# Performance work log

Measured on AMD Instinct MI355X. Metric: run time of the kernel, lower is better.

## Reference

```python
import jax, jax.numpy as jnp
import numpy as np

ANCHORS = np.array([[10,13],[16,30],[33,23],[30,61],[62,45],[59,119],[116,90],[156,198],[373,326]], dtype=np.float32)
STRIDES = [32, 16, 8]
GROUPS = [2, 1, 0]  # anchor_masks [[6,7,8],[3,4,5],[0,1,2]] -> group index = mask[0]//3
N_CLASSES = 80
IGNORE_THRESH = 0.7


def _safe_log(x):
    # replicates torch BCELoss log clamp at -100, NaN-safe under grad
    ok = x > 0
    return jnp.where(ok, jnp.log(jnp.where(ok, x, 1.0)), -100.0)


def _bce_sum(o, t, w=None):
    l = -(t * _safe_log(o) + (1.0 - t) * _safe_log(1.0 - o))
    if w is not None:
        l = l * w
    return jnp.sum(l)


def _layer_loss(raw, labels, stride, group):
    dtype = raw.dtype
    B, C, H, W = raw.shape
    nch = 5 + N_CLASSES
    A = 3
    fsize = H
    T = labels.shape[1]
    all_grid = jnp.asarray(ANCHORS).astype(dtype) / stride          # [9,2] anchors in grid units
    manch = all_grid[3 * group:3 * group + 3]                        # [3,2]

    # ---- make_pred ----
    o = raw.reshape(B, A, nch, H, W).transpose(0, 1, 3, 4, 2)        # [B,A,H,W,nch]
    out = jnp.concatenate([jax.nn.sigmoid(o[..., :2]), o[..., 2:4], jax.nn.sigmoid(o[..., 4:])], axis=-1)
    xs = jnp.arange(W, dtype=dtype)
    ys = jnp.arange(H, dtype=dtype)
    px = out[..., 0] + xs                                            # broadcast over W
    py = out[..., 1] + ys[:, None]
    pw = jnp.exp(o[..., 2]) * manch[:, 0][:, None, None]
    ph = jnp.exp(o[..., 3]) * manch[:, 1][:, None, None]
    pred = jnp.stack([px, py, pw, ph], axis=-1)                      # [B,A,H,W,4] (cx,cy,w,h)

    # ---- truths ----
    tx = labels[..., 1] * fsize
    ty = labels[..., 2] * fsize
    tw = labels[..., 3] * fsize
    th = labels[..., 4] * fsize
    valid = jnp.sum(labels, axis=-1) > 0                             # [B,T]
    gi = tx.astype(jnp.int32)                                        # truncation (coords >= 0)
    gj = ty.astype(jnp.int32)

    # ---- anchor matching: aligned-wh IoU vs all 9 anchors ----
    mw = jnp.minimum(tw[..., None], all_grid[:, 0])                  # [B,T,9]
    mh = jnp.minimum(th[..., None], all_grid[:, 1])
    en = ((mw > 0) & (mh > 0)).astype(dtype)
    inter = mw * mh * en
    a_iou = inter / (tw[..., None] * th[..., None] + all_grid[:, 0] * all_grid[:, 1] - inter)
    best_all = jnp.argmax(a_iou, axis=-1)                            # [B,T]
    best_n = best_all % 3
    sel = valid & ((best_all // 3) == group)

    # ---- ignore mask from pred IoU (xywh) ----
    predf = pred.reshape(B, -1, 4)                                   # [B,N,4], N=A*H*W
    truth = jnp.stack([tx, ty, tw, th], axis=-1)                     # [B,T,4]
    a_tl = predf[:, :, None, :2] - predf[:, :, None, 2:] * 0.5
    a_br = predf[:, :, None, :2] + predf[:, :, None, 2:] * 0.5
    b_tl = truth[:, None, :, :2] - truth[:, None, :, 2:] * 0.5
    b_br = truth[:, None, :, :2] + truth[:, None, :, 2:] * 0.5
    tl = jnp.maximum(a_tl, b_tl)
    br = jnp.minimum(a_br, b_br)
    enp = jnp.all(tl < br, axis=-1).astype(dtype)
    ai = jnp.prod(br - tl, axis=-1) * enp                            # [B,N,T]
    area_a = predf[:, :, 2] * predf[:, :, 3]
    area_b = truth[:, :, 2] * truth[:, :, 3]
    piou = ai / (area_a[:, :, None] + area_b[:, None, :] - ai)
    piou = jnp.where(valid[:, None, :], piou, 0.0)
    obj_mask = (~(jnp.max(piou, axis=-1) > IGNORE_THRESH)).astype(dtype).reshape(B, A, H, W)

    # ---- scatter matched targets (unmatched routed OOB and dropped) ----
    bidx = jnp.broadcast_to(jnp.arange(B)[:, None], (B, T))
    a_s = jnp.where(sel, best_n, A)                                  # A is out of bounds -> dropped
    obj_mask = obj_mask.at[bidx, a_s, gj, gi].set(1.0, mode='drop')
    tm1 = jnp.zeros((B, A, H, W), dtype).at[bidx, a_s, gj, gi].set(1.0, mode='drop')
    scale = jnp.sqrt(2.0 - tw * th / float(fsize * fsize))
    ts1 = jnp.zeros((B, A, H, W), dtype).at[bidx, a_s, gj, gi].set(scale, mode='drop')

    aw = manch[best_n, 0]
    ah = manch[best_n, 1]
    onehot = jax.nn.one_hot(labels[..., 0].astype(jnp.int32), N_CLASSES, dtype=dtype)
    v = jnp.concatenate([
        (tx - gi.astype(dtype))[..., None],
        (ty - gj.astype(dtype))[..., None],
        jnp.log(tw / aw + 1e-16)[..., None],
        jnp.log(th / ah + 1e-16)[..., None],
        jnp.ones_like(tx)[..., None],
        onehot,
    ], axis=-1)                                                      # [B,T,nch]
    target = jnp.zeros((B, A, H, W, nch), dtype).at[bidx, a_s, gj, gi].set(v, mode='drop')

    # ---- losses ----
    tm = tm1[..., None]
    ts = ts1[..., None]
    o_xy = out[..., :2] * tm
    t_xy = target[..., :2] * tm
    o_wh = out[..., 2:4] * tm * ts
    t_wh = target[..., 2:4] * tm * ts
    o_ob = out[..., 4] * obj_mask
    t_ob = target[..., 4] * obj_mask
    o_cl = out[..., 5:] * tm
    t_cl = target[..., 5:] * tm

    loss_xy = _bce_sum(o_xy, t_xy, ts * ts)
    loss_wh = 0.5 * jnp.sum((o_wh - t_wh) ** 2)
    loss_obj = _bce_sum(o_ob, t_ob)
    loss_cls = _bce_sum(o_cl, t_cl)
    return loss_xy + loss_wh + loss_obj + loss_cls


def setup_inputs() -> dict:
    key = jax.random.key(0)
    ks = jax.random.split(key, 7)
    B, T = 16, 50
    out0 = jax.random.normal(ks[0], (B, 255, 19, 19), jnp.float32)
    out1 = jax.random.normal(ks[1], (B, 255, 38, 38), jnp.float32)
    out2 = jax.random.normal(ks[2], (B, 255, 76, 76), jnp.float32)
    cls = jax.random.randint(ks[3], (B, T, 1), 0, N_CLASSES).astype(jnp.float32)
    xy = jax.random.uniform(ks[4], (B, T, 2), jnp.float32, 0.1, 0.9)
    wh = jax.random.uniform(ks[5], (B, T, 2), jnp.float32, 0.05, 0.3)
    labels = jnp.concatenate([cls, xy, wh], axis=-1)
    nvalid = jax.random.randint(ks[6], (B, 1), 1, T + 1)
    vmask = (jnp.arange(T)[None, :] < nvalid).astype(jnp.float32)
    targets = labels * vmask[..., None]                              # padded rows are all-zero
    return {"out0": out0, "out1": out1, "out2": out2, "targets": targets}


def reference(out0, out1, out2, targets):
    outs = [out0, out1, out2]
    total = jnp.zeros((), outs[0].dtype)
    for layer in range(3):
        total = total + _layer_loss(outs[layer], targets, STRIDES[layer], GROUPS[layer])
    return total
```

## Files before the change

### kernel.cpp

```cpp
#include <hip/hip_runtime.h>
#include <math.h>

#define T_TGT 50
#define NCLS 80
#define NBATCH 16

#define NB_L0 5
#define NB_L1 17
#define NB_L2 68
#define NB_MAIN ((NB_L0 + NB_L1 + NB_L2) * NBATCH)
#define N_CLS_UNITS (T_TGT * NBATCH * 3)
#define NB_CLS ((N_CLS_UNITS + 3) / 4)
#define NB_TOTAL (NB_MAIN + NB_CLS)


__constant__ float c_anchors[18] = {10,13,16,30,33,23,30,61,62,45,
                                    59,119,116,90,156,198,373,326};

__device__ __forceinline__ float softplusf(float x){
    return fmaxf(x, 0.f) + log1pf(expf(-fabsf(x)));
}
__device__ __forceinline__ float bcef(float x, float t){
    return t * softplusf(-x) + (1.f - t) * softplusf(x);
}

struct SmemMain {
    float4 box[T_TGT];
    float  thr[T_TGT];
    float  fx[T_TGT];
    float  fy[T_TGT];
    float  lw[T_TGT];
    float  lh[T_TGT];
    float  w2[T_TGT];
    int    win[256];
    int    nval;
};

template<int H, int STRIDE, int GROUP>
__device__ float main_cells(const float* __restrict__ raw,
                            const float* __restrict__ targets,
                            int b, int cb, int tid, SmemMain* sm)
{
    constexpr int HH = H * H;
    constexpr int CELLS = 3 * HH;

    const int c = cb * 256 + tid;
    const bool cell_ok = (c < CELLS);
    int a = 0, j = 0, i = 0;
    float x0 = 0.f, x1 = 0.f, x2 = 0.f, x3 = 0.f, x4 = 0.f;
    if (cell_ok) {
        a = c / HH;
        const int rem = c - a * HH;
        j = rem / H;
        i = rem - j * H;
        const float* base = raw + ((size_t)b * 255 + a * 85) * HH + rem;
        x0 = base[0];
        x1 = base[HH];
        x2 = base[2 * HH];
        x3 = base[3 * HH];
        x4 = base[4 * HH];
    }

    sm->win[tid] = -1;

    bool scat = false; int rel = 0;
    if (tid < 64) {
        bool valid = false;
        float tx = 0.f, ty = 0.f, tw = 0.f, th = 0.f, tarea = 0.f;
        int bestn = 0;
        if (tid < T_TGT) {
            const float* lab = targets + ((size_t)b * T_TGT + tid) * 5;
            float cf = lab[0], x = lab[1], y = lab[2], w = lab[3], h = lab[4];
            valid = (cf + x + y + w + h) > 0.f;
            const float fs = (float)H;
            tx = x * fs; ty = y * fs; tw = w * fs; th = h * fs;
            tarea = tw * th;
            float best = -1.f;
            #pragma unroll
            for (int n = 0; n < 9; n++) {
                float aw = c_anchors[2*n]   * (1.f / STRIDE);
                float ah = c_anchors[2*n+1] * (1.f / STRIDE);
                float mw = fminf(tw, aw), mh = fminf(th, ah);
                float inter = (mw > 0.f && mh > 0.f) ? mw * mh : 0.f;
                float iou = inter / (tarea + aw * ah - inter);
                if (iou > best) { best = iou; bestn = n; }
            }
        }
        const unsigned long long vm = __ballot(valid);
        if (valid) {
            const int idx = __popcll(vm & ((1ull << tid) - 1ull));
            sm->box[idx] = make_float4(tx - tw*0.5f, ty - th*0.5f,
                                       tx + tw*0.5f, ty + th*0.5f);
            sm->thr[idx] = 0.7f * tarea;
            const int gi = (int)tx, gj = (int)ty;
            sm->fx[tid] = tx - (float)gi;
            sm->fy[tid] = ty - (float)gj;
            const int bn = bestn % 3;
            const float awm = c_anchors[2*(3*GROUP + bn)]   * (1.f / STRIDE);
            const float ahm = c_anchors[2*(3*GROUP + bn)+1] * (1.f / STRIDE);
            sm->lw[tid] = logf(tw / awm + 1e-16f);
            sm->lh[tid] = logf(th / ahm + 1e-16f);
            sm->w2[tid] = 2.f - tarea / ((float)H * (float)H);
            if (((bestn / 3) == GROUP) &&
                ((unsigned)gi < (unsigned)H) && ((unsigned)gj < (unsigned)H)) {
                const int ct = bn * HH + gj * H + gi;
                rel = ct - cb * 256;
                scat = (rel >= 0) && (rel < 256);
            }
        }
        if (tid == 0) sm->nval = __popcll(vm);
    }
    __syncthreads();
    if (scat) atomicMax(&sm->win[rel], tid);
    __syncthreads();

    float local = 0.f;
    const int winner = sm->win[tid];

    float atlx = 0.f, atly = 0.f, abrx = 0.f, abry = 0.f, carea_a = 0.f;
    if (cell_ok) {
        const float s0 = 1.f / (1.f + expf(-x0));
        const float s1 = 1.f / (1.f + expf(-x1));
        const float manw = c_anchors[2*(3*GROUP + a)]   * (1.f / STRIDE);
        const float manh = c_anchors[2*(3*GROUP + a)+1] * (1.f / STRIDE);
        const float px = s0 + (float)i, py = s1 + (float)j;
        const float pw = expf(x2) * manw, ph = expf(x3) * manh;
        atlx = px - pw * 0.5f; atly = py - ph * 0.5f;
        abrx = px + pw * 0.5f; abry = py + ph * 0.5f;
        carea_a = 0.7f * (pw * ph);
    }

    bool ign = (!cell_ok) || (winner >= 0);
    const int nval = sm->nval;

    #define IGN_BODY(tt) {                                          \
        const float4 bx = sm->box[tt];                              \
        const float thr = sm->thr[tt];                              \
        const float tlx = fmaxf(atlx, bx.x);                        \
        const float tly = fmaxf(atly, bx.y);                        \
        const float brx = fminf(abrx, bx.z);                        \
        const float bry = fminf(abry, bx.w);                        \
        const float dx = brx - tlx, dy = bry - tly;                 \
        ign = ign || ((fminf(dx, dy) > 0.f) &&                      \
                      (fmaf(1.7f, dx * dy, -carea_a) > thr)); }

    int t = 0;
    while (t + 4 <= nval) {
        if (__all(ign)) break;
        IGN_BODY(t) IGN_BODY(t+1) IGN_BODY(t+2) IGN_BODY(t+3)
        t += 4;
    }
    if (!__all(ign))
        for (; t < nval; ++t) IGN_BODY(t)
    #undef IGN_BODY

    if (winner >= 0) {
        local += softplusf(-x4);
        const float w2v = sm->w2[winner];
        local += w2v * (bcef(x0, sm->fx[winner]) + bcef(x1, sm->fy[winner]));
        const float dw = x2 - sm->lw[winner];
        const float dh = x3 - sm->lh[winner];
        local += 0.5f * w2v * (dw * dw + dh * dh);
    } else if (!ign) {
        local += softplusf(x4);
    }
    return local;
}

__device__ float class_unit(const float* __restrict__ r0,
                            const float* __restrict__ r1,
                            const float* __restrict__ r2,
                            const float* __restrict__ targets,
                            int u, int lane)
{
    const int L   = u / (T_TGT * NBATCH);
    const int rem = u - L * (T_TGT * NBATCH);
    const int b   = rem / T_TGT;
    const int t0  = rem - b * T_TGT;

    const int Hs[3] = {19, 38, 76};
    const float inv_s[3] = {1.f/32.f, 1.f/16.f, 1.f/8.f};
    const int Gs[3] = {2, 1, 0};
    const float* raw = (L == 0) ? r0 : (L == 1) ? r1 : r2;
    const int H = Hs[L];
    const int HH = H * H;
    const float is = inv_s[L];
    const int group = Gs[L];

    int selkey = 0x40000000 | lane;
    int clsid = 0;
    if (lane < T_TGT) {
        const float* lab = targets + ((size_t)b * T_TGT + lane) * 5;
        float cf = lab[0], x = lab[1], y = lab[2], w = lab[3], h = lab[4];
        bool valid = (cf + x + y + w + h) > 0.f;
        float fs = (float)H;
        float tx = x * fs, ty = y * fs, tw = w * fs, th = h * fs;
        float tarea = tw * th;
        float best = -1.f; int bestn = 0;
        #pragma unroll
        for (int n = 0; n < 9; n++) {
            float aw = c_anchors[2*n] * is, ah = c_anchors[2*n+1] * is;
            float mw = fminf(tw, aw), mh = fminf(th, ah);
            float inter = (mw > 0.f && mh > 0.f) ? mw * mh : 0.f;
            float iou = inter / (tarea + aw * ah - inter);
            if (iou > best) { best = iou; bestn = n; }
        }
        if (valid && (bestn / 3) == group) {
            int bn = bestn % 3, gi = (int)tx, gj = (int)ty;
            selkey = (bn << 20) | (gj << 10) | gi;
        }
        clsid = (int)cf;
    }

    const int k0 = __shfl(selkey, t0);
    bool active = !(k0 & 0x40000000);
    unsigned long long dup = __ballot(selkey == k0);
    active = active && !(dup >> (t0 + 1));

    float local = 0.f;
    if (active) {
        const int cls0 = __shfl(clsid, t0);
        const int gi = k0 & 1023, gj = (k0 >> 10) & 1023, bn = k0 >> 20;
        const float* base = raw + ((size_t)b * 255 + bn * 85) * HH + gj * H + gi;
        float xc = base[(size_t)(5 + lane) * HH];
        local = softplusf(xc) - ((lane == cls0) ? xc : 0.f);
        if (lane < 16) {
            float xh = base[(size_t)(69 + lane) * HH];
            local += softplusf(xh) - ((lane + 64 == cls0) ? xh : 0.f);
        }
    }
    return local;
}

__global__ __launch_bounds__(256)
void yolo_fused(const float* __restrict__ r0,
                const float* __restrict__ r1,
                const float* __restrict__ r2,
                const float* __restrict__ targets,
                float* __restrict__ partial)
{
    __shared__ SmemMain sm;
    __shared__ float s_wsum[4];

    const int blk = blockIdx.x;
    const int tid = threadIdx.x;
    float local = 0.f;

    if (blk < NB_L0 * NBATCH) {
        int b = blk / NB_L0, cb = blk - b * NB_L0;
        local = main_cells<19, 32, 2>(r0, targets, b, cb, tid, &sm);
    } else if (blk < (NB_L0 + NB_L1) * NBATCH) {
        int q = blk - NB_L0 * NBATCH;
        int b = q / NB_L1, cb = q - b * NB_L1;
        local = main_cells<38, 16, 1>(r1, targets, b, cb, tid, &sm);
    } else if (blk < NB_MAIN) {
        int q = blk - (NB_L0 + NB_L1) * NBATCH;
        int b = q / NB_L2, cb = q - b * NB_L2;
        local = main_cells<76, 8, 0>(r2, targets, b, cb, tid, &sm);
    } else {
        int u = (blk - NB_MAIN) * 4 + (tid >> 6);
        if (u < N_CLS_UNITS)
            local = class_unit(r0, r1, r2, targets, u, tid & 63);
    }

    for (int off = 32; off > 0; off >>= 1)
        local += __shfl_down(local, off, 64);
    const int lane = tid & 63, wv = tid >> 6;
    if (lane == 0) s_wsum[wv] = local;
    __syncthreads();
    if (tid == 0)
        partial[blk] = s_wsum[0] + s_wsum[1] + s_wsum[2] + s_wsum[3];
}

__global__ __launch_bounds__(256)
void yolo_reduce(const float4* __restrict__ partial4, float* __restrict__ out)
{
    const int tid = threadIdx.x;
    constexpr int NV = NB_TOTAL / 4;
    float4 v = partial4[tid];
    float s = v.x + v.y + v.z + v.w;
    if (tid + 256 < NV) {
        float4 u = partial4[tid + 256];
        s += u.x + u.y + u.z + u.w;
    }
    for (int off = 32; off > 0; off >>= 1)
        s += __shfl_down(s, off, 64);
    __shared__ float w[4];
    if ((tid & 63) == 0) w[tid >> 6] = s;
    __syncthreads();
    if (tid == 0) out[0] = w[0] + w[1] + w[2] + w[3];
}

extern "C" void kernel_launch(void* const* d_in, const int* in_sizes, int n_in,
                              void* d_out, int out_size, void* d_ws, size_t ws_size,
                              hipStream_t stream)
{
    const float* out0 = (const float*)d_in[0];
    const float* out1 = (const float*)d_in[1];
    const float* out2 = (const float*)d_in[2];
    const float* tgt  = (const float*)d_in[3];
    float* out = (float*)d_out;
    float* partial = (float*)d_ws;

    yolo_fused<<<NB_TOTAL, 256, 0, stream>>>(out0, out1, out2, tgt, partial);
    yolo_reduce<<<1, 256, 0, stream>>>((const float4*)partial, out);
}
```

Measured before the change: 148.0 us.

## Fold class loss into main cell kernel and process two cells per thread

Removes the separate class-loss blocks. Each winner cell now computes its 80-class BCE inside the main-cell epilogue, using a class id kept in shared memory. Main blocks now cover 512 cells each, two per thread, which halves the block count and shares the per-block target setup and ignore-loop box loads across two cells. The cost is a serial, strided 80-element loop in the few winner threads, which diverges from the rest of the wavefront, plus higher register use from carrying two cells' state.

```diff
diff --git a/kernel.cpp b/kernel.cpp
--- a/kernel.cpp
+++ b/kernel.cpp
@@ -5,13 +5,11 @@
 #define NCLS 80
 #define NBATCH 16
 
-#define NB_L0 5
-#define NB_L1 17
-#define NB_L2 68
+#define NB_L0 3
+#define NB_L1 9
+#define NB_L2 34
 #define NB_MAIN ((NB_L0 + NB_L1 + NB_L2) * NBATCH)
-#define N_CLS_UNITS (T_TGT * NBATCH * 3)
-#define NB_CLS ((N_CLS_UNITS + 3) / 4)
-#define NB_TOTAL (NB_MAIN + NB_CLS)
+#define NB_TOTAL NB_MAIN
 
 
 __constant__ float c_anchors[18] = {10,13,16,30,33,23,30,61,62,45,
@@ -27,12 +25,11 @@
 struct SmemMain {
     float4 box[T_TGT];
     float  thr[T_TGT];
-    float  fx[T_TGT];
-    float  fy[T_TGT];
-    float  lw[T_TGT];
-    float  lh[T_TGT];
+    float2 fxy[T_TGT];
+    float2 lwh[T_TGT];
     float  w2[T_TGT];
-    int    win[256];
+    int    cls[T_TGT];
+    int    win[512];
     int    nval;
 };
 
@@ -44,24 +41,29 @@
     constexpr int HH = H * H;
     constexpr int CELLS = 3 * HH;
 
-    const int c = cb * 256 + tid;
-    const bool cell_ok = (c < CELLS);
-    int a = 0, j = 0, i = 0;
-    float x0 = 0.f, x1 = 0.f, x2 = 0.f, x3 = 0.f, x4 = 0.f;
-    if (cell_ok) {
-        a = c / HH;
-        const int rem = c - a * HH;
-        j = rem / H;
-        i = rem - j * H;
-        const float* base = raw + ((size_t)b * 255 + a * 85) * HH + rem;
-        x0 = base[0];
-        x1 = base[HH];
-        x2 = base[2 * HH];
-        x3 = base[3 * HH];
-        x4 = base[4 * HH];
+    const int c0 = cb * 512 + tid;
+    const int c1 = c0 + 256;
+    const bool ok0 = (c0 < CELLS);
+    const bool ok1 = (c1 < CELLS);
+    int a0 = 0, j0 = 0, i0 = 0, rem0 = 0;
+    int a1 = 0, j1 = 0, i1 = 0, rem1 = 0;
+    float y00=0.f, y01=0.f, y02=0.f, y03=0.f, y04=0.f;
+    float y10=0.f, y11=0.f, y12=0.f, y13=0.f, y14=0.f;
+    if (ok0) {
+        a0 = c0 / HH; rem0 = c0 - a0 * HH; j0 = rem0 / H; i0 = rem0 - j0 * H;
+        const float* base = raw + ((size_t)b * 255 + a0 * 85) * HH + rem0;
+        y00 = base[0]; y01 = base[HH]; y02 = base[2*HH];
+        y03 = base[3*HH]; y04 = base[4*HH];
+    }
+    if (ok1) {
+        a1 = c1 / HH; rem1 = c1 - a1 * HH; j1 = rem1 / H; i1 = rem1 - j1 * H;
+        const float* base = raw + ((size_t)b * 255 + a1 * 85) * HH + rem1;
+        y10 = base[0]; y11 = base[HH]; y12 = base[2*HH];
+        y13 = base[3*HH]; y14 = base[4*HH];
     }
 
     sm->win[tid] = -1;
+    sm->win[tid + 256] = -1;
 
     bool scat = false; int rel = 0;
     if (tid < 64) {
@@ -85,6 +87,7 @@
                 float iou = inter / (tarea + aw * ah - inter);
                 if (iou > best) { best = iou; bestn = n; }
             }
+            sm->cls[tid] = (int)cf;
         }
         const unsigned long long vm = __ballot(valid);
         if (valid) {
@@ -93,19 +96,18 @@
                                        tx + tw*0.5f, ty + th*0.5f);
             sm->thr[idx] = 0.7f * tarea;
             const int gi = (int)tx, gj = (int)ty;
-            sm->fx[tid] = tx - (float)gi;
-            sm->fy[tid] = ty - (float)gj;
+            sm->fxy[tid] = make_float2(tx - (float)gi, ty - (float)gj);
             const int bn = bestn % 3;
             const float awm = c_anchors[2*(3*GROUP + bn)]   * (1.f / STRIDE);
             const float ahm = c_anchors[2*(3*GROUP + bn)+1] * (1.f / STRIDE);
-            sm->lw[tid] = logf(tw / awm + 1e-16f);
-            sm->lh[tid] = logf(th / ahm + 1e-16f);
+            sm->lwh[tid] = make_float2(logf(tw / awm + 1e-16f),
+                                       logf(th / ahm + 1e-16f));
             sm->w2[tid] = 2.f - tarea / ((float)H * (float)H);
             if (((bestn / 3) == GROUP) &&
                 ((unsigned)gi < (unsigned)H) && ((unsigned)gj < (unsigned)H)) {
                 const int ct = bn * HH + gj * H + gi;
-                rel = ct - cb * 256;
-                scat = (rel >= 0) && (rel < 256);
+                rel = ct - cb * 512;
+                scat = (rel >= 0) && (rel < 512);
             }
         }
         if (tid == 0) sm->nval = __popcll(vm);
@@ -114,121 +116,93 @@
     if (scat) atomicMax(&sm->win[rel], tid);
     __syncthreads();
 
-    float local = 0.f;
-    const int winner = sm->win[tid];
-
-    float atlx = 0.f, atly = 0.f, abrx = 0.f, abry = 0.f, carea_a = 0.f;
-    if (cell_ok) {
-        const float s0 = 1.f / (1.f + expf(-x0));
-        const float s1 = 1.f / (1.f + expf(-x1));
-        const float manw = c_anchors[2*(3*GROUP + a)]   * (1.f / STRIDE);
-        const float manh = c_anchors[2*(3*GROUP + a)+1] * (1.f / STRIDE);
-        const float px = s0 + (float)i, py = s1 + (float)j;
-        const float pw = expf(x2) * manw, ph = expf(x3) * manh;
-        atlx = px - pw * 0.5f; atly = py - ph * 0.5f;
-        abrx = px + pw * 0.5f; abry = py + ph * 0.5f;
-        carea_a = 0.7f * (pw * ph);
-    }
-
-    bool ign = (!cell_ok) || (winner >= 0);
+    const int w0 = sm->win[tid];
+    const int w1 = sm->win[tid + 256];
     const int nval = sm->nval;
+
+    float atlx0=0.f, atly0=0.f, abrx0=0.f, abry0=0.f, ca0=0.f;
+    float atlx1=0.f, atly1=0.f, abrx1=0.f, abry1=0.f, ca1=0.f;
+    if (ok0) {
+        const float s0 = 1.f / (1.f + expf(-y00));
+        const float s1 = 1.f / (1.f + expf(-y01));
+        const float mw = c_anchors[2*(3*GROUP + a0)]   * (1.f / STRIDE);
+        const float mh = c_anchors[2*(3*GROUP + a0)+1] * (1.f / STRIDE);
+        const float px = s0 + (float)i0, py = s1 + (float)j0;
+        const float pw = expf(y02) * mw, ph = expf(y03) * mh;
+        atlx0 = px - pw*0.5f; atly0 = py - ph*0.5f;
+        abrx0 = px + pw*0.5f; abry0 = py + ph*0.5f;
+        ca0 = 0.7f * (pw * ph);
+    }
+    if (ok1) {
+        const float s0 = 1.f / (1.f + expf(-y10));
+        const float s1 = 1.f / (1.f + expf(-y11));
+        const float mw = c_anchors[2*(3*GROUP + a1)]   * (1.f / STRIDE);
+        const float mh = c_anchors[2*(3*GROUP + a1)+1] * (1.f / STRIDE);
+        const float px = s0 + (float)i1, py = s1 + (float)j1;
+        const float pw = expf(y12) * mw, ph = expf(y13) * mh;
+        atlx1 = px - pw*0.5f; atly1 = py - ph*0.5f;
+        abrx1 = px + pw*0.5f; abry1 = py + ph*0.5f;
+        ca1 = 0.7f * (pw * ph);
+    }
+
+    bool ign0 = (!ok0) || (w0 >= 0);
+    bool ign1 = (!ok1) || (w1 >= 0);
 
     #define IGN_BODY(tt) {                                          \
         const float4 bx = sm->box[tt];                              \
         const float thr = sm->thr[tt];                              \
-        const float tlx = fmaxf(atlx, bx.x);                        \
-        const float tly = fmaxf(atly, bx.y);                        \
-        const float brx = fminf(abrx, bx.z);                        \
-        const float bry = fminf(abry, bx.w);                        \
-        const float dx = brx - tlx, dy = bry - tly;                 \
-        ign = ign || ((fminf(dx, dy) > 0.f) &&                      \
-                      (fmaf(1.7f, dx * dy, -carea_a) > thr)); }
+        float tlx = fmaxf(atlx0, bx.x);                             \
+        float tly = fmaxf(atly0, bx.y);                             \
+        float brx = fminf(abrx0, bx.z);                             \
+        float bry = fminf(abry0, bx.w);                             \
+        float dx = brx - tlx, dy = bry - tly;                       \
+        ign0 = ign0 || ((fminf(dx, dy) > 0.f) &&                    \
+                        (fmaf(1.7f, dx * dy, -ca0) > thr));         \
+        tlx = fmaxf(atlx1, bx.x);                                   \
+        tly = fmaxf(atly1, bx.y);                                   \
+        brx = fminf(abrx1, bx.z);                                   \
+        bry = fminf(abry1, bx.w);                                   \
+        dx = brx - tlx; dy = bry - tly;                             \
+        ign1 = ign1 || ((fminf(dx, dy) > 0.f) &&                    \
+                        (fmaf(1.7f, dx * dy, -ca1) > thr)); }
 
     int t = 0;
-    while (t + 4 <= nval) {
-        if (__all(ign)) break;
+    bool done = __all(ign0 && ign1);
+    while (!done && t + 4 <= nval) {
         IGN_BODY(t) IGN_BODY(t+1) IGN_BODY(t+2) IGN_BODY(t+3)
         t += 4;
-    }
-    if (!__all(ign))
+        done = __all(ign0 && ign1);
+    }
+    if (!done)
         for (; t < nval; ++t) IGN_BODY(t)
     #undef IGN_BODY
 
-    if (winner >= 0) {
-        local += softplusf(-x4);
-        const float w2v = sm->w2[winner];
-        local += w2v * (bcef(x0, sm->fx[winner]) + bcef(x1, sm->fy[winner]));
-        const float dw = x2 - sm->lw[winner];
-        const float dh = x3 - sm->lh[winner];
-        local += 0.5f * w2v * (dw * dw + dh * dh);
-    } else if (!ign) {
-        local += softplusf(x4);
-    }
-    return local;
-}
-
-__device__ float class_unit(const float* __restrict__ r0,
-                            const float* __restrict__ r1,
-                            const float* __restrict__ r2,
-                            const float* __restrict__ targets,
-                            int u, int lane)
-{
-    const int L   = u / (T_TGT * NBATCH);
-    const int rem = u - L * (T_TGT * NBATCH);
-    const int b   = rem / T_TGT;
-    const int t0  = rem - b * T_TGT;
-
-    const int Hs[3] = {19, 38, 76};
-    const float inv_s[3] = {1.f/32.f, 1.f/16.f, 1.f/8.f};
-    const int Gs[3] = {2, 1, 0};
-    const float* raw = (L == 0) ? r0 : (L == 1) ? r1 : r2;
-    const int H = Hs[L];
-    const int HH = H * H;
-    const float is = inv_s[L];
-    const int group = Gs[L];
-
-    int selkey = 0x40000000 | lane;
-    int clsid = 0;
-    if (lane < T_TGT) {
-        const float* lab = targets + ((size_t)b * T_TGT + lane) * 5;
-        float cf = lab[0], x = lab[1], y = lab[2], w = lab[3], h = lab[4];
-        bool valid = (cf + x + y + w + h) > 0.f;
-        float fs = (float)H;
-        float tx = x * fs, ty = y * fs, tw = w * fs, th = h * fs;
-        float tarea = tw * th;
-        float best = -1.f; int bestn = 0;
-        #pragma unroll
-        for (int n = 0; n < 9; n++) {
-            float aw = c_anchors[2*n] * is, ah = c_anchors[2*n+1] * is;
-            float mw = fminf(tw, aw), mh = fminf(th, ah);
-            float inter = (mw > 0.f && mh > 0.f) ? mw * mh : 0.f;
-            float iou = inter / (tarea + aw * ah - inter);
-            if (iou > best) { best = iou; bestn = n; }
-        }
-        if (valid && (bestn / 3) == group) {
-            int bn = bestn % 3, gi = (int)tx, gj = (int)ty;
-            selkey = (bn << 20) | (gj << 10) | gi;
-        }
-        clsid = (int)cf;
-    }
-
-    const int k0 = __shfl(selkey, t0);
-    bool active = !(k0 & 0x40000000);
-    unsigned long long dup = __ballot(selkey == k0);
-    active = active && !(dup >> (t0 + 1));
-
     float local = 0.f;
-    if (active) {
-        const int cls0 = __shfl(clsid, t0);
-        const int gi = k0 & 1023, gj = (k0 >> 10) & 1023, bn = k0 >> 20;
-        const float* base = raw + ((size_t)b * 255 + bn * 85) * HH + gj * H + gi;
-        float xc = base[(size_t)(5 + lane) * HH];
-        local = softplusf(xc) - ((lane == cls0) ? xc : 0.f);
-        if (lane < 16) {
-            float xh = base[(size_t)(69 + lane) * HH];
-            local += softplusf(xh) - ((lane + 64 == cls0) ? xh : 0.f);
-        }
-    }
+
+    #define EPILOGUE(w, ign, x0, x1, x2, x3, x4, aa, rr) {              \
+        if (w >= 0) {                                                   \
+            local += softplusf(-(x4));                                  \
+            const float w2v = sm->w2[w];                                \
+            const float2 f = sm->fxy[w];                                \
+            local += w2v * (bcef(x0, f.x) + bcef(x1, f.y));             \
+            const float2 lw = sm->lwh[w];                               \
+            const float dw = (x2) - lw.x, dh = (x3) - lw.y;             \
+            local += 0.5f * w2v * (dw * dw + dh * dh);                  \
+            const int cls = sm->cls[w];                                 \
+            const float* cb_ = raw + ((size_t)b*255 + (aa)*85 + 5)*HH + (rr); \
+            float cl = 0.f;                                             \
+            _Pragma("unroll 20")                                        \
+            for (int cc = 0; cc < NCLS; cc++)                           \
+                cl += softplusf(cb_[(size_t)cc * HH]);                  \
+            local += cl - cb_[(size_t)cls * HH];                        \
+        } else if (!(ign)) {                                            \
+            local += softplusf(x4);                                     \
+        } }
+
+    EPILOGUE(w0, ign0, y00, y01, y02, y03, y04, a0, rem0)
+    EPILOGUE(w1, ign1, y10, y11, y12, y13, y14, a1, rem1)
+    #undef EPILOGUE
+
     return local;
 }
 
@@ -253,14 +227,10 @@
         int q = blk - NB_L0 * NBATCH;
         int b = q / NB_L1, cb = q - b * NB_L1;
         local = main_cells<38, 16, 1>(r1, targets, b, cb, tid, &sm);
-    } else if (blk < NB_MAIN) {
+    } else {
         int q = blk - (NB_L0 + NB_L1) * NBATCH;
         int b = q / NB_L2, cb = q - b * NB_L2;
         local = main_cells<76, 8, 0>(r2, targets, b, cb, tid, &sm);
-    } else {
-        int u = (blk - NB_MAIN) * 4 + (tid >> 6);
-        if (u < N_CLS_UNITS)
-            local = class_unit(r0, r1, r2, targets, u, tid & 63);
     }
 
     for (int off = 32; off > 0; off >>= 1)
@@ -277,11 +247,10 @@
 {
     const int tid = threadIdx.x;
     constexpr int NV = NB_TOTAL / 4;
-    float4 v = partial4[tid];
-    float s = v.x + v.y + v.z + v.w;
-    if (tid + 256 < NV) {
-        float4 u = partial4[tid + 256];
-        s += u.x + u.y + u.z + u.w;
+    float s = 0.f;
+    if (tid < NV) {
+        float4 v = partial4[tid];
+        s = v.x + v.y + v.z + v.w;
     }
     for (int off = 32; off > 0; off >>= 1)
         s += __shfl_down(s, off, 64);
```

New measurement: 311.6 us. 2.11x slower.
